# Kernel tuning notes

Measured on AMD Instinct MI355X. Metric: run time of the kernel, lower is better.

The kernel has to match this reference:

```python
import jax, jax.numpy as jnp
import numpy as np

B, S, H, N, D, R = 2, 2048, 768, 12, 64, 5  # batch, seq, hidden, heads, head_dim, n_structural_deps


def setup_inputs() -> dict:
    key = jax.random.key(0)
    ks = jax.random.split(key, 12)
    hidden_states = jax.random.normal(ks[0], (B, S, H), dtype=jnp.float32)
    attention_mask = jnp.zeros((B, 1, 1, S), dtype=jnp.float32)  # additive mask, all-visible
    # binary structural adjacency per dependency, broadcast over heads
    graph_adj = (jax.random.uniform(ks[1], (R, B, 1, S, S)) < 0.1).astype(jnp.float32)
    s = 0.02
    Wq = jax.random.normal(ks[2], (H, H), dtype=jnp.float32) * s
    bq = jnp.zeros((H,), dtype=jnp.float32)
    Wk = jax.random.normal(ks[3], (H, H), dtype=jnp.float32) * s
    bk = jnp.zeros((H,), dtype=jnp.float32)
    Wv = jax.random.normal(ks[4], (H, H), dtype=jnp.float32) * s
    bv = jnp.zeros((H,), dtype=jnp.float32)
    # biaffine bilinear forms, one [N, D, D] per structural dependency
    bili = jax.random.normal(ks[5], (R, N, D, D), dtype=jnp.float32) * s
    abs_bias = jnp.zeros((R, N), dtype=jnp.float32)  # initialized to zeros as in torch
    return {
        'hidden_states': hidden_states, 'attention_mask': attention_mask,
        'graph_adj': graph_adj, 'Wq': Wq, 'bq': bq, 'Wk': Wk, 'bk': bk,
        'Wv': Wv, 'bv': bv, 'bili': bili, 'abs_bias': abs_bias, 'layer_idx': 0,
    }


def reference(hidden_states, attention_mask, graph_adj, Wq, bq, Wk, bk, Wv, bv,
              bili, abs_bias, layer_idx):
    b, s, h = hidden_states.shape
    n, d = N, D

    def heads(x):  # [b, s, h] -> [b, n, s, d]
        return x.reshape(b, s, n, d).transpose(0, 2, 1, 3)

    q = heads(hidden_states @ Wq.T + bq)
    k = heads(hidden_states @ Wk.T + bk)
    v = heads(hidden_states @ Wv.T + bv)

    scores = jnp.einsum('bnid,bnjd->bnij', q, k)  # [b, n, s, s]
    # biaffine structural bias per dependency, masked by graph adjacency
    for i in range(R):  # small fixed structural loop
        bias = jnp.einsum('bnip,npq,bnjq->bnij', q, bili[i], k)
        bias = bias + abs_bias[i][None, :, None, None]
        scores = scores + bias * graph_adj[i]

    scores = scores / np.sqrt(d).astype(np.float32) + attention_mask
    probs = jax.nn.softmax(scores, axis=-1)
    ctx = jnp.einsum('bnij,bnjd->bnid', probs, v)  # [b, n, s, d]
    return ctx.transpose(0, 2, 1, 3).reshape(b, s, h)
```

## Files before the change

### kernel.cpp

```cpp
#include <hip/hip_runtime.h>
#include <cstdint>
#include <cstddef>

#define B_  2
#define S_  2048
#define H_  768
#define NH  12
#define DH  64
#define RD  5
#define BN  (B_*NH)

typedef _Float16 f16;
typedef __attribute__((ext_vector_type(8))) _Float16 f16x8;
typedef __attribute__((ext_vector_type(4))) float f32x4;

#define MFMA16(a, b, c) __builtin_amdgcn_mfma_f32_16x16x32_f16((a), (b), (c), 0, 0, 0)

#if __has_builtin(__builtin_amdgcn_exp2f)
__device__ __forceinline__ float exp2fast(float x) { return __builtin_amdgcn_exp2f(x); }
#else
__device__ __forceinline__ float exp2fast(float x) { return __expf(0.69314718056f * x); }
#endif

#define SCL 0.1803368801f
#define L2E 1.44269504f

__device__ __forceinline__ void cvt16(const float* __restrict__ src, f16* dst)
{
    float4 f0 = ((const float4*)src)[0];
    float4 f1 = ((const float4*)src)[1];
    float4 f2 = ((const float4*)src)[2];
    float4 f3 = ((const float4*)src)[3];
    f16 h[16] = {(f16)f0.x, (f16)f0.y, (f16)f0.z, (f16)f0.w,
                 (f16)f1.x, (f16)f1.y, (f16)f1.z, (f16)f1.w,
                 (f16)f2.x, (f16)f2.y, (f16)f2.z, (f16)f2.w,
                 (f16)f3.x, (f16)f3.y, (f16)f3.z, (f16)f3.w};
    *(f16x8*)dst       = *(const f16x8*)&h[0];
    *(f16x8*)(dst + 8) = *(const f16x8*)&h[8];
}

__global__ __launch_bounds__(256, 3) void qkv_pack(
    const float* __restrict__ hs,
    const float* __restrict__ Wq, const float* __restrict__ Wk,
    const float* __restrict__ Wv,
    const float* __restrict__ bq, const float* __restrict__ bk,
    const float* __restrict__ bv,
    f16* __restrict__ qo, f16* __restrict__ ko, f16* __restrict__ vt,
    const float* __restrict__ adj, unsigned char* __restrict__ adjp)
{
    __shared__ __align__(16) f16 Xs[64][72];
    __shared__ __align__(16) f16 Ws[3][64][72];

    const int tid = threadIdx.x;

    if (blockIdx.x >= 768) {
        const int idx4 = (blockIdx.x - 768) * 256 + tid;
        const int j4 = idx4 & 511;
        const int iq = (idx4 >> 9) & 511;
        const int b  = idx4 >> 18;
        unsigned int wbits[4] = {0, 0, 0, 0};
#pragma unroll
        for (int r = 0; r < RD; ++r) {
#pragma unroll
            for (int ii = 0; ii < 4; ++ii) {
                float4 v = *(const float4*)(adj +
                    (((size_t)(r * B_ + b) * S_) + iq * 4 + ii) * S_ + j4 * 4);
                float vv[4] = {v.x, v.y, v.z, v.w};
#pragma unroll
                for (int jj = 0; jj < 4; ++jj)
                    wbits[jj] |= (vv[jj] != 0.f ? 1u : 0u) << (r + 8 * ii);
            }
        }
        uint4 pk = {wbits[0], wbits[1], wbits[2], wbits[3]};
        *(uint4*)(adjp + ((size_t)(b * 512 + iq) * S_ + j4 * 4) * 4) = pk;
        return;
    }

    const int n  = blockIdx.x % 12;
    const int m0 = (blockIdx.x / 12) * 64;
    const int w = tid >> 6, lane = tid & 63;
    const int l15 = lane & 15, quad = lane >> 4;
    const int srow = tid >> 2, sc0 = (tid & 3) * 16;

    f32x4 acc[3][4];
#pragma unroll
    for (int i = 0; i < 3; ++i)
#pragma unroll
        for (int ns = 0; ns < 4; ++ns) acc[i][ns] = (f32x4){0.f, 0.f, 0.f, 0.f};

    const float* xsrc = hs + (size_t)(m0 + srow) * H_ + sc0;
    const float* w0src = Wq + (size_t)(n * 64 + srow) * H_ + sc0;
    const float* w1src = Wk + (size_t)(n * 64 + srow) * H_ + sc0;
    const float* w2src = Wv + (size_t)(n * 64 + srow) * H_ + sc0;

    for (int kc = 0; kc < 12; ++kc) {
        __syncthreads();
        cvt16(xsrc  + kc * 64, &Xs[srow][sc0]);
        cvt16(w0src + kc * 64, &Ws[0][srow][sc0]);
        cvt16(w1src + kc * 64, &Ws[1][srow][sc0]);
        cvt16(w2src + kc * 64, &Ws[2][srow][sc0]);
        __syncthreads();

        f16x8 a0 = *(const f16x8*)&Xs[w * 16 + l15][quad * 8];
        f16x8 a1 = *(const f16x8*)&Xs[w * 16 + l15][quad * 8 + 32];
#pragma unroll
        for (int i = 0; i < 3; ++i)
#pragma unroll
            for (int ns = 0; ns < 4; ++ns) {
                f16x8 b0 = *(const f16x8*)&Ws[i][ns * 16 + l15][quad * 8];
                f16x8 b1 = *(const f16x8*)&Ws[i][ns * 16 + l15][quad * 8 + 32];
                acc[i][ns] = MFMA16(a0, b0, acc[i][ns]);
                acc[i][ns] = MFMA16(a1, b1, acc[i][ns]);
            }
    }
    __syncthreads();

    const float* bias[3] = {bq, bk, bv};
    f16 (*T0)[72] = Xs;
    f16 (*T1)[72] = Ws[0];
    f16 (*T2)[72] = Ws[1];
#pragma unroll
    for (int i = 0; i < 3; ++i) {
        f16 (*T)[72] = (i == 0) ? T0 : (i == 1) ? T1 : T2;
#pragma unroll
        for (int ns = 0; ns < 4; ++ns) {
            float bb = bias[i][n * 64 + ns * 16 + l15];
#pragma unroll
            for (int reg = 0; reg < 4; ++reg)
                T[w * 16 + quad * 4 + reg][ns * 16 + l15] =
                    (f16)(acc[i][ns][reg] + bb);
        }
    }
    __syncthreads();

    const int mrow = m0 + srow;
    const int bb2 = mrow >> 11, ss = mrow & 2047;
    {
        f16* dst = qo + ((size_t)(bb2 * NH + n) * S_ + ss) * DH + sc0;
        *(f16x8*)dst       = *(const f16x8*)&T0[srow][sc0];
        *(f16x8*)(dst + 8) = *(const f16x8*)&T0[srow][sc0 + 8];
    }
    {
        f16* dst = ko + ((size_t)(bb2 * NH + n) * S_ + ss) * DH + sc0;
        *(f16x8*)dst       = *(const f16x8*)&T1[srow][sc0];
        *(f16x8*)(dst + 8) = *(const f16x8*)&T1[srow][sc0 + 8];
    }
    {
        f16 tmp[16];
#pragma unroll
        for (int u = 0; u < 16; ++u) tmp[u] = T2[sc0 + u][srow];
        f16* dst = vt + ((size_t)(bb2 * NH + n) * DH + srow) * S_ + (m0 & 2047) + sc0;
        *(f16x8*)dst       = *(const f16x8*)&tmp[0];
        *(f16x8*)(dst + 8) = *(const f16x8*)&tmp[8];
    }
}

__global__ __launch_bounds__(256, 3) void qprime(
    const f16* __restrict__ q, const float* __restrict__ bili,
    f16* __restrict__ qp)
{
    __shared__ __align__(16) f16 Mt[64 * 72];
    __shared__ __align__(16) f16 Pb[4 * 16 * 72];

    const int tid = threadIdx.x;
    const int idx = blockIdx.x;
    const int it = idx & 31;
    const int bn = idx >> 5;
    const int n = bn % NH;
    const int w = tid >> 6, lane = tid & 63;
    const int l15 = lane & 15, quad = lane >> 4;
    const int wi0 = it * 64 + w * 16;
    const size_t kbase = (size_t)bn * S_ * DH;

    const f16* qrow = q + kbase + (size_t)(wi0 + l15) * DH + quad * 8;
    f16x8 aq0 = *(const f16x8*)(qrow);
    f16x8 aq1 = *(const f16x8*)(qrow + 32);

    f16* Pw = Pb + w * 16 * 72;

#pragma unroll
    for (int r = 0; r < RD; ++r) {
        __syncthreads();
        {
            int p = tid >> 2, q0 = (tid & 3) * 16;
            const float* src = bili + ((size_t)(r * NH + n) * DH + p) * DH + q0;
            float4 g0 = ((const float4*)src)[0];
            float4 g1 = ((const float4*)src)[1];
            float4 g2 = ((const float4*)src)[2];
            float4 g3 = ((const float4*)src)[3];
            float mv[16] = {g0.x, g0.y, g0.z, g0.w, g1.x, g1.y, g1.z, g1.w,
                            g2.x, g2.y, g2.z, g2.w, g3.x, g3.y, g3.z, g3.w};
#pragma unroll
            for (int u = 0; u < 16; ++u) Mt[(q0 + u) * 72 + p] = (f16)mv[u];
        }
        __syncthreads();
#pragma unroll
        for (int ns = 0; ns < 4; ++ns) {
            f16x8 b0 = *(const f16x8*)&Mt[(ns * 16 + l15) * 72 + quad * 8];
            f16x8 b1 = *(const f16x8*)&Mt[(ns * 16 + l15) * 72 + quad * 8 + 32];
            f32x4 d = {0.f, 0.f, 0.f, 0.f};
            d = MFMA16(aq0, b0, d);
            d = MFMA16(aq1, b1, d);
#pragma unroll
            for (int reg = 0; reg < 4; ++reg)
                Pw[(quad * 4 + reg) * 72 + ns * 16 + l15] = (f16)d[reg];
        }
        f16x8 v0 = *(const f16x8*)&Pw[l15 * 72 + quad * 8];
        f16x8 v1 = *(const f16x8*)&Pw[l15 * 72 + quad * 8 + 32];
        f16* dst = qp + ((size_t)(bn * RD + r) * S_ + wi0 + l15) * 64 + quad * 8;
        *(f16x8*)dst        = v0;
        *(f16x8*)(dst + 32) = v1;
    }
}

__global__ __launch_bounds__(256, 4) void attn(
    const f16* __restrict__ q, const f16* __restrict__ k, const f16* __restrict__ vt,
    const f16* __restrict__ qp, const unsigned char* __restrict__ adjp,
    const float* __restrict__ mask, const float* __restrict__ absb,
    float* __restrict__ po, float* __restrict__ pm, float* __restrict__ pl)
{
    __shared__ __align__(16) char smem[9216 + 128];
    f16*   Pb  = (f16*)smem;
    float* lut = (float*)(smem + 9216);

    const int tid = threadIdx.x;
    const int idx = blockIdx.x;
    const int g = idx & 7;
    const int it = (idx >> 3) & 31;
    const int half = (idx >> 8) & 1;
    const int bn = 8 * (idx >> 9) + g;
    const int b = bn / NH, n = bn % NH;
    const int w = tid >> 6, lane = tid & 63;
    const int l15 = lane & 15, quad = lane >> 4;
    const int wi0 = it * 64 + w * 16;
    const size_t kbase = (size_t)bn * S_ * DH;

    if (tid < 32) {
        float a = 0.f;
#pragma unroll
        for (int r = 0; r < RD; ++r)
            if (tid & (1 << r)) a += absb[r * NH + n];
        lut[tid] = a * SCL;
    }
    __syncthreads();

    const f16* qrow = q + kbase + (size_t)(wi0 + l15) * DH + quad * 8;
    f16x8 aq0 = *(const f16x8*)(qrow);
    f16x8 aq1 = *(const f16x8*)(qrow + 32);

    f16x8 aqp[RD][2];
    {
        const f16* qpb = qp + ((size_t)(bn * RD) * S_ + wi0 + l15) * 64 + quad * 8;
#pragma unroll
        for (int r = 0; r < RD; ++r) {
            aqp[r][0] = *(const f16x8*)(qpb + (size_t)r * S_ * 64);
            aqp[r][1] = *(const f16x8*)(qpb + (size_t)r * S_ * 64 + 32);
        }
    }

    f16* Pw = Pb + w * 16 * 72;

    f16x8 ones;
#pragma unroll
    for (int u = 0; u < 8; ++u) ones[u] = (f16)1.0f;

    f32x4 o[4] = {{0,0,0,0},{0,0,0,0},{0,0,0,0},{0,0,0,0}};
    f32x4 lacc = {0.f, 0.f, 0.f, 0.f};
    float mrun[4] = {-1e30f, -1e30f, -1e30f, -1e30f};

    const unsigned char* adjrow =
        adjp + (size_t)(b * 512 + (wi0 >> 2) + quad) * (S_ * 4);
    const float* maskrow = mask + (size_t)b * S_;
    const f16* vtb = vt + (size_t)bn * DH * S_;

    const int t0 = half * 16;
#pragma unroll 1
    for (int t = t0; t < t0 + 16; ++t) {
        const int j0 = t * 64;
        float sc[4][4];

#pragma unroll
        for (int js = 0; js < 4; ++js) {
            const int jcol = j0 + js * 16 + l15;
            const f16* kp = k + kbase + (size_t)jcol * DH + quad * 8;
            f16x8 bk0 = *(const f16x8*)(kp);
            f16x8 bk1 = *(const f16x8*)(kp + 32);

            f32x4 aqk = {0.f, 0.f, 0.f, 0.f};
            aqk = MFMA16(aq0, bk0, aqk);
            aqk = MFMA16(aq1, bk1, aqk);

            uchar4 a4 = *(const uchar4*)(adjrow + (size_t)jcol * 4);
            unsigned int bbits[4] = {a4.x, a4.y, a4.z, a4.w};
            float mkL = maskrow[jcol] * L2E;

            float s0 = aqk[0], s1 = aqk[1], s2 = aqk[2], s3 = aqk[3];
#pragma unroll
            for (int r = 0; r < RD; ++r) {
                f32x4 z = {0.f, 0.f, 0.f, 0.f};
                z = MFMA16(aqp[r][0], bk0, z);
                z = MFMA16(aqp[r][1], bk1, z);
                s0 = fmaf((float)((bbits[0] >> r) & 1u), z[0], s0);
                s1 = fmaf((float)((bbits[1] >> r) & 1u), z[1], s1);
                s2 = fmaf((float)((bbits[2] >> r) & 1u), z[2], s2);
                s3 = fmaf((float)((bbits[3] >> r) & 1u), z[3], s3);
            }
            sc[js][0] = fmaf(s0, SCL, lut[bbits[0]] + mkL);
            sc[js][1] = fmaf(s1, SCL, lut[bbits[1]] + mkL);
            sc[js][2] = fmaf(s2, SCL, lut[bbits[2]] + mkL);
            sc[js][3] = fmaf(s3, SCL, lut[bbits[3]] + mkL);
        }

        float alpha[4];
#pragma unroll
        for (int reg = 0; reg < 4; ++reg) {
            float nm = fmaxf(fmaxf(sc[0][reg], sc[1][reg]),
                             fmaxf(sc[2][reg], sc[3][reg]));
#pragma unroll
            for (int off = 1; off < 16; off <<= 1)
                nm = fmaxf(nm, __shfl_xor(nm, off));
            float mn = fmaxf(mrun[reg], nm);
            alpha[reg] = exp2fast(mrun[reg] - mn);
            mrun[reg] = mn;
        }
#pragma unroll
        for (int js = 0; js < 4; ++js)
#pragma unroll
            for (int reg = 0; reg < 4; ++reg) {
                float p = exp2fast(sc[js][reg] - mrun[reg]);
                Pw[(quad * 4 + reg) * 72 + js * 16 + l15] = (f16)p;
            }
#pragma unroll
        for (int reg = 0; reg < 4; ++reg) {
            lacc[reg] *= alpha[reg];
#pragma unroll
            for (int ds = 0; ds < 4; ++ds) o[ds][reg] *= alpha[reg];
        }

        f16x8 pa0 = *(const f16x8*)&Pw[l15 * 72 + quad * 8];
        f16x8 pa1 = *(const f16x8*)&Pw[l15 * 72 + quad * 8 + 32];
        lacc = MFMA16(pa0, ones, lacc);
        lacc = MFMA16(pa1, ones, lacc);
#pragma unroll
        for (int ds = 0; ds < 4; ++ds) {
            const f16* vp = vtb + (size_t)(ds * 16 + l15) * S_ + j0 + quad * 8;
            f16x8 bv0 = *(const f16x8*)(vp);
            f16x8 bv1 = *(const f16x8*)(vp + 32);
            o[ds] = MFMA16(pa0, bv0, o[ds]);
            o[ds] = MFMA16(pa1, bv1, o[ds]);
        }
    }

    const size_t rbase = (size_t)(half * BN + bn) * S_;
#pragma unroll
    for (int reg = 0; reg < 4; ++reg) {
        int i = wi0 + quad * 4 + reg;
        float* prow = po + (rbase + i) * 64;
#pragma unroll
        for (int ds = 0; ds < 4; ++ds)
            prow[ds * 16 + l15] = o[ds][reg];
        if (l15 == 0) {
            pm[rbase + i] = mrun[reg];
            pl[rbase + i] = lacc[reg];
        }
    }
}

__global__ __launch_bounds__(256) void merge(
    const float* __restrict__ po, const float* __restrict__ pm,
    const float* __restrict__ pl, float* __restrict__ out)
{
    const int t = blockIdx.x * 256 + threadIdx.x;
    const int rid = t >> 4;
    const int d4 = t & 15;
    const int bn = rid >> 11, row = rid & 2047;
    const int b = bn / NH, n = bn % NH;

    const float m0 = pm[rid], m1 = pm[BN * S_ + rid];
    const float l0 = pl[rid], l1 = pl[BN * S_ + rid];
    const float mN = fmaxf(m0, m1);
    const float c0 = exp2fast(m0 - mN), c1 = exp2fast(m1 - mN);
    const float inv = 1.f / (l0 * c0 + l1 * c1);

    const float4 o0 = ((const float4*)po)[(size_t)rid * 16 + d4];
    const float4 o1 = ((const float4*)po)[((size_t)BN * S_ + rid) * 16 + d4];
    float4 r;
    r.x = (o0.x * c0 + o1.x * c1) * inv;
    r.y = (o0.y * c0 + o1.y * c1) * inv;
    r.z = (o0.z * c0 + o1.z * c1) * inv;
    r.w = (o0.w * c0 + o1.w * c1) * inv;
    ((float4*)out)[(size_t)(b * S_ + row) * (H_ / 4) + n * (DH / 4) + d4] = r;
}

extern "C" void kernel_launch(void* const* d_in, const int* in_sizes, int n_in,
                              void* d_out, int out_size, void* d_ws, size_t ws_size,
                              hipStream_t stream)
{
    const float* hs   = (const float*)d_in[0];
    const float* mask = (const float*)d_in[1];
    const float* adj  = (const float*)d_in[2];
    const float* Wq   = (const float*)d_in[3];
    const float* bq   = (const float*)d_in[4];
    const float* Wk   = (const float*)d_in[5];
    const float* bk   = (const float*)d_in[6];
    const float* Wv   = (const float*)d_in[7];
    const float* bv   = (const float*)d_in[8];
    const float* bili = (const float*)d_in[9];
    const float* absb = (const float*)d_in[10];
    float* out = (float*)d_out;

    const size_t QKV = (size_t)BN * S_ * DH;
    f16* q  = (f16*)d_ws;
    f16* k  = q + QKV;
    f16* vt = k + QKV;
    unsigned char* adjp = (unsigned char*)(vt + QKV);
    f16* qp = (f16*)(adjp + (size_t)B_ * 512 * S_ * 4);
    float* po = (float*)(qp + (size_t)RD * QKV);
    float* pm = po + (size_t)2 * BN * S_ * DH;
    float* pl = pm + (size_t)2 * BN * S_;

    qkv_pack<<<768 + 2048, 256, 0, stream>>>(hs, Wq, Wk, Wv, bq, bk, bv,
                                             q, k, vt, adj, adjp);
    qprime<<<768, 256, 0, stream>>>(q, bili, qp);
    attn<<<1536, 256, 0, stream>>>(q, k, vt, qp, adjp, mask, absb, po, pm, pl);
    merge<<<3072, 256, 0, stream>>>(po, pm, pl, out);
}
```

Baseline: 572.7 us.

## Use single-wave attention blocks over full key range and drop split-K merge

The attention kernel now launches one 64-thread block per 16-row query tile and iterates over all 32 key tiles, instead of four waves per block each covering half the keys. Each block normalizes and writes its output directly, so the partial-output buffers and the separate merge kernel go away. This removes the extra global round trip and one kernel launch, but halves the number of waves in flight and makes each wave's loop twice as long. The syncthreads after the LUT setup is dropped, which is safe only because the block is now a single wave.

```diff
diff --git a/kernel.cpp b/kernel.cpp
--- a/kernel.cpp
+++ b/kernel.cpp
@@ -213,25 +213,23 @@
     }
 }
 
-__global__ __launch_bounds__(256, 4) void attn(
+__global__ __launch_bounds__(64, 5) void attn(
     const f16* __restrict__ q, const f16* __restrict__ k, const f16* __restrict__ vt,
     const f16* __restrict__ qp, const unsigned char* __restrict__ adjp,
     const float* __restrict__ mask, const float* __restrict__ absb,
-    float* __restrict__ po, float* __restrict__ pm, float* __restrict__ pl)
-{
-    __shared__ __align__(16) char smem[9216 + 128];
-    f16*   Pb  = (f16*)smem;
-    float* lut = (float*)(smem + 9216);
+    float* __restrict__ out)
+{
+    __shared__ __align__(16) f16 Pw[16 * 72];
+    __shared__ float lut[32];
 
     const int tid = threadIdx.x;
     const int idx = blockIdx.x;
     const int g = idx & 7;
     const int it = (idx >> 3) & 31;
-    const int half = (idx >> 8) & 1;
-    const int bn = 8 * (idx >> 9) + g;
+    const int w = (idx >> 8) & 3;
+    const int bn = 8 * (idx >> 10) + g;
     const int b = bn / NH, n = bn % NH;
-    const int w = tid >> 6, lane = tid & 63;
-    const int l15 = lane & 15, quad = lane >> 4;
+    const int l15 = tid & 15, quad = tid >> 4;
     const int wi0 = it * 64 + w * 16;
     const size_t kbase = (size_t)bn * S_ * DH;
 
@@ -242,7 +240,6 @@
             if (tid & (1 << r)) a += absb[r * NH + n];
         lut[tid] = a * SCL;
     }
-    __syncthreads();
 
     const f16* qrow = q + kbase + (size_t)(wi0 + l15) * DH + quad * 8;
     f16x8 aq0 = *(const f16x8*)(qrow);
@@ -257,8 +254,6 @@
             aqp[r][1] = *(const f16x8*)(qpb + (size_t)r * S_ * 64 + 32);
         }
     }
-
-    f16* Pw = Pb + w * 16 * 72;
 
     f16x8 ones;
 #pragma unroll
@@ -273,9 +268,8 @@
     const float* maskrow = mask + (size_t)b * S_;
     const f16* vtb = vt + (size_t)bn * DH * S_;
 
-    const int t0 = half * 16;
 #pragma unroll 1
-    for (int t = t0; t < t0 + 16; ++t) {
+    for (int t = 0; t < 32; ++t) {
         const int j0 = t * 64;
         float sc[4][4];
 
@@ -351,45 +345,15 @@
         }
     }
 
-    const size_t rbase = (size_t)(half * BN + bn) * S_;
 #pragma unroll
     for (int reg = 0; reg < 4; ++reg) {
+        float inv = 1.f / lacc[reg];
         int i = wi0 + quad * 4 + reg;
-        float* prow = po + (rbase + i) * 64;
 #pragma unroll
         for (int ds = 0; ds < 4; ++ds)
-            prow[ds * 16 + l15] = o[ds][reg];
-        if (l15 == 0) {
-            pm[rbase + i] = mrun[reg];
-            pl[rbase + i] = lacc[reg];
-        }
-    }
-}
-
-__global__ __launch_bounds__(256) void merge(
-    const float* __restrict__ po, const float* __restrict__ pm,
-    const float* __restrict__ pl, float* __restrict__ out)
-{
-    const int t = blockIdx.x * 256 + threadIdx.x;
-    const int rid = t >> 4;
-    const int d4 = t & 15;
-    const int bn = rid >> 11, row = rid & 2047;
-    const int b = bn / NH, n = bn % NH;
-
-    const float m0 = pm[rid], m1 = pm[BN * S_ + rid];
-    const float l0 = pl[rid], l1 = pl[BN * S_ + rid];
-    const float mN = fmaxf(m0, m1);
-    const float c0 = exp2fast(m0 - mN), c1 = exp2fast(m1 - mN);
-    const float inv = 1.f / (l0 * c0 + l1 * c1);
-
-    const float4 o0 = ((const float4*)po)[(size_t)rid * 16 + d4];
-    const float4 o1 = ((const float4*)po)[((size_t)BN * S_ + rid) * 16 + d4];
-    float4 r;
-    r.x = (o0.x * c0 + o1.x * c1) * inv;
-    r.y = (o0.y * c0 + o1.y * c1) * inv;
-    r.z = (o0.z * c0 + o1.z * c1) * inv;
-    r.w = (o0.w * c0 + o1.w * c1) * inv;
-    ((float4*)out)[(size_t)(b * S_ + row) * (H_ / 4) + n * (DH / 4) + d4] = r;
+            out[((size_t)b * S_ + i) * H_ + n * DH + ds * 16 + l15] =
+                o[ds][reg] * inv;
+    }
 }
 
 extern "C" void kernel_launch(void* const* d_in, const int* in_sizes, int n_in,
@@ -415,13 +379,9 @@
     f16* vt = k + QKV;
     unsigned char* adjp = (unsigned char*)(vt + QKV);
     f16* qp = (f16*)(adjp + (size_t)B_ * 512 * S_ * 4);
-    float* po = (float*)(qp + (size_t)RD * QKV);
-    float* pm = po + (size_t)2 * BN * S_ * DH;
-    float* pl = pm + (size_t)2 * BN * S_;
 
     qkv_pack<<<768 + 2048, 256, 0, stream>>>(hs, Wq, Wk, Wv, bq, bk, bv,
                                              q, k, vt, adj, adjp);
     qprime<<<768, 256, 0, stream>>>(q, bili, qp);
-    attn<<<1536, 256, 0, stream>>>(q, k, vt, qp, adjp, mask, absb, po, pm, pl);
-    merge<<<3072, 256, 0, stream>>>(po, pm, pl, out);
-}
+    attn<<<3072, 64, 0, stream>>>(q, k, vt, qp, adjp, mask, absb, out);
+}
```

Result: slower. 658.6 us (+15.0%).
